# Kernel optimization log

Hardware: AMD Instinct MI355X
Metric: run time of the kernel (lower is better)

The kernel has to match this reference:

```python
import jax, jax.numpy as jnp
import numpy as np

D_MODEL = 1024
N_HEADS = 16
D_K = D_MODEL // N_HEADS
NEG = -1e9


def setup_inputs() -> dict:
    key = jax.random.key(0)
    ks = jax.random.split(key, 10)
    B, S = 4, 2048
    x = jax.random.normal(ks[0], (B, S, D_MODEL), dtype=jnp.float32)
    mask = jax.random.randint(ks[1], (B, S, S), 0, 2).astype(jnp.bool_)
    sc = 1.0 / np.sqrt(D_MODEL)
    Wq = jax.random.normal(ks[2], (D_MODEL, D_MODEL), dtype=jnp.float32) * sc
    bq = jnp.zeros((D_MODEL,), dtype=jnp.float32)
    Wk = jax.random.normal(ks[3], (D_MODEL, D_MODEL), dtype=jnp.float32) * sc
    bk = jnp.zeros((D_MODEL,), dtype=jnp.float32)
    Wv = jax.random.normal(ks[4], (D_MODEL, D_MODEL), dtype=jnp.float32) * sc
    bv = jnp.zeros((D_MODEL,), dtype=jnp.float32)
    Wo = jax.random.normal(ks[5], (D_MODEL, D_MODEL), dtype=jnp.float32) * sc
    bo = jnp.zeros((D_MODEL,), dtype=jnp.float32)
    return {"x": x, "mask": mask, "Wq": Wq, "bq": bq, "Wk": Wk, "bk": bk,
            "Wv": Wv, "bv": bv, "Wo": Wo, "bo": bo}


def _split_heads(t, B, S):
    # [B,S,d_model] -> [B,H,S,d_k]
    return t.reshape(B, S, N_HEADS, D_K).transpose(0, 2, 1, 3)


def reference(x, mask, Wq, bq, Wk, bk, Wv, bv, Wo, bo):
    B, S, _ = x.shape
    Q = _split_heads(x @ Wq + bq, B, S)
    K = _split_heads(x @ Wk + bk, B, S)
    V = _split_heads(x @ Wv + bv, B, S)
    scale = jnp.sqrt(jnp.float32(D_K))
    scores = jnp.einsum('bhqd,bhkd->bhqk', Q, K) / scale
    scores = jnp.where(mask[:, None, :, :], jnp.float32(NEG), scores)
    attn = jax.nn.softmax(scores, axis=-1)
    ctx = jnp.einsum('bhqk,bhkd->bhqd', attn, V)
    ctx = ctx.transpose(0, 2, 1, 3).reshape(B, S, D_MODEL)
    return ctx @ Wo + bo
```

## Files before the change

### kernel.cpp

```cpp
#include <hip/hip_runtime.h>

#define D_MODEL 1024
#define N_HEADS 16
#define D_K     64
#define BATCH   4
#define SEQ     2048
#define MROWS   (BATCH * SEQ)
#define QSCALE  0.18033688011112042f

typedef __bf16 bf16x8 __attribute__((ext_vector_type(8)));
typedef float  f32x4  __attribute__((ext_vector_type(4)));
typedef float  f32x16 __attribute__((ext_vector_type(16)));
typedef unsigned short ushort8 __attribute__((ext_vector_type(8)));
typedef unsigned short ushort4v __attribute__((ext_vector_type(4)));

#if __has_builtin(__builtin_amdgcn_exp2f)
#define EXP2F(x) __builtin_amdgcn_exp2f(x)
#else
#define EXP2F(x) exp2f(x)
#endif

#define CVT_PK_BF16(d, a, b) \
    asm("v_cvt_pk_bf16_f32 %0, %1, %2" : "=v"(d) : "v"(a), "v"(b))
#define PERMSWAP(a, b) \
    asm("v_permlane32_swap_b32 %0, %1" : "+v"(a), "+v"(b))
#define WAIT_VM(N) asm volatile("s_waitcnt vmcnt(" #N ")" ::: "memory")
#define CFENCE()   asm volatile("" ::: "memory")

__device__ inline unsigned short f2bf(float f) {
    union { float f; unsigned int u; } v; v.f = f;
    unsigned int u = v.u;
    unsigned int r = (u + 0x7fffu + ((u >> 16) & 1u)) >> 16;
    return (unsigned short)r;
}

__device__ inline void load_lds16(const void* g, void* l) {
    __builtin_amdgcn_global_load_lds(
        (const __attribute__((address_space(1))) unsigned int*)g,
        (__attribute__((address_space(3))) unsigned int*)l, 16, 0, 0);
}

__global__ __launch_bounds__(256) void wprep(const float* __restrict__ Wq,
                                             const float* __restrict__ Wk,
                                             const float* __restrict__ Wv,
                                             const float* __restrict__ Wo,
                                             unsigned short* __restrict__ wt) {
    __shared__ __align__(16) unsigned short t[64][65];
    int w  = blockIdx.z;
    const float* W = (w == 0) ? Wq : (w == 1) ? Wk : (w == 2) ? Wv : Wo;
    int k0 = blockIdx.x * 64, n0 = blockIdx.y * 64;
    int tid = threadIdx.x;
    int nl = tid & 63, kq = tid >> 6;
#pragma unroll
    for (int i = 0; i < 16; i++) {
        int kl = kq * 16 + i;
        t[kl][nl] = f2bf(W[(size_t)(k0 + kl) * D_MODEL + n0 + nl]);
    }
    __syncthreads();
    unsigned short* out = wt + (size_t)w * D_MODEL * D_MODEL;
#pragma unroll
    for (int p = 0; p < 2; p++) {
        int nrow = p * 32 + (tid >> 3);
        int c8   = (tid & 7) * 8;
        ushort8 o;
#pragma unroll
        for (int j = 0; j < 8; j++) o[j] = t[c8 + j][nrow];
        *reinterpret_cast<ushort8*>(out + (size_t)(n0 + nrow) * D_MODEL + k0 + c8) = o;
    }
}

__global__ __launch_bounds__(256) void xprep(const float4* __restrict__ x,
                                             unsigned short* __restrict__ xb) {
    int i = blockIdx.x * 256 + threadIdx.x;
    float4 v = x[i];
    ushort4v o;
    o[0] = f2bf(v.x); o[1] = f2bf(v.y); o[2] = f2bf(v.z); o[3] = f2bf(v.w);
    *reinterpret_cast<ushort4v*>(xb + (size_t)i * 4) = o;
}

__global__ __launch_bounds__(256) void mprep(const int* __restrict__ mask,
                                             unsigned long long* __restrict__ mb) {
    int row = blockIdx.x;
    int tid = threadIdx.x;
    int wv  = tid >> 6;
#pragma unroll
    for (int w = 0; w < 8; w++) {
        int col = w * 256 + tid;
        int mval = mask[(size_t)row * SEQ + col];
        unsigned long long bits = __ballot(mval != 0);
        if ((tid & 63) == 0) mb[(size_t)row * 32 + w * 4 + wv] = bits;
    }
}

__global__ __launch_bounds__(256) void qkv_gemm(const unsigned short* __restrict__ xb,
                                                const unsigned short* __restrict__ wt,
                                                const float* __restrict__ bq,
                                                const float* __restrict__ bk,
                                                const float* __restrict__ bvv,
                                                unsigned short* __restrict__ qb,
                                                unsigned short* __restrict__ kb,
                                                unsigned short* __restrict__ vt) {
    __shared__ __align__(16) unsigned short lds_a[128 * 32];
    __shared__ __align__(16) unsigned short lds_b[128 * 32];
    int tid = threadIdx.x;
    int wave = tid >> 6, lane = tid & 63;
    int c = lane & 15, g = lane >> 4;
    int wave_m = (wave & 1) * 64, wave_n = (wave >> 1) * 64;
    int nblk = blockIdx.x * 128, mblk = blockIdx.y * 128;

    int oct0 = wave * 128 + lane, oct1 = oct0 + 64;
    int ra0 = oct0 >> 2, ga0 = ((oct0 & 3) ^ (ra0 & 3)) * 8;
    int ra1 = oct1 >> 2, ga1 = ((oct1 & 3) ^ (ra1 & 3)) * 8;
    const unsigned short* pa0 = xb + (size_t)(mblk + ra0) * D_MODEL + ga0;
    const unsigned short* pa1 = xb + (size_t)(mblk + ra1) * D_MODEL + ga1;
    const unsigned short* pb0 = wt + (size_t)(nblk + ra0) * D_MODEL + ga0;
    const unsigned short* pb1 = wt + (size_t)(nblk + ra1) * D_MODEL + ga1;
    unsigned short* la0 = lds_a + wave * 1024;
    unsigned short* la1 = la0 + 512;
    unsigned short* lb0 = lds_b + wave * 1024;
    unsigned short* lb1 = lb0 + 512;

    int aoff[4], boff[4];
#pragma unroll
    for (int mi = 0; mi < 4; mi++) {
        int row = wave_m + mi * 16 + c;
        aoff[mi] = (row * 4 + (g ^ (row & 3))) * 16;
    }
#pragma unroll
    for (int ni = 0; ni < 4; ni++) {
        int row = wave_n + ni * 16 + c;
        boff[ni] = (row * 4 + (g ^ (row & 3))) * 16;
    }

    f32x4 acc[4][4];
#pragma unroll
    for (int mi = 0; mi < 4; mi++)
#pragma unroll
        for (int ni = 0; ni < 4; ni++) acc[mi][ni] = f32x4{0.f, 0.f, 0.f, 0.f};

    for (int k0 = 0; k0 < D_MODEL; k0 += 32) {
        load_lds16(pa0 + k0, la0);
        load_lds16(pa1 + k0, la1);
        load_lds16(pb0 + k0, lb0);
        load_lds16(pb1 + k0, lb1);
        __syncthreads();
        bf16x8 af[4], bfr[4];
#pragma unroll
        for (int mi = 0; mi < 4; mi++)
            af[mi] = *reinterpret_cast<const bf16x8*>(reinterpret_cast<const char*>(lds_a) + aoff[mi]);
#pragma unroll
        for (int ni = 0; ni < 4; ni++)
            bfr[ni] = *reinterpret_cast<const bf16x8*>(reinterpret_cast<const char*>(lds_b) + boff[ni]);
#pragma unroll
        for (int mi = 0; mi < 4; mi++)
#pragma unroll
            for (int ni = 0; ni < 4; ni++)
                acc[mi][ni] = __builtin_amdgcn_mfma_f32_16x16x32_bf16(af[mi], bfr[ni], acc[mi][ni], 0, 0, 0);
        __syncthreads();
    }

    int nb = nblk + wave_n;
    int wsel = nb >> 10;
    int h = (nb >> 6) & 15;
    int dk0 = nb & 63;
    int mglob = mblk + wave_m;
    int b = mglob >> 11;
    int s0 = mglob & (SEQ - 1);
    size_t bh = (size_t)(b * N_HEADS + h);
    const float* bias = (wsel == 0) ? bq : (wsel == 1) ? bk : bvv;
    int nn = nb & (D_MODEL - 1);
    float bval[4];
#pragma unroll
    for (int ni = 0; ni < 4; ni++) bval[ni] = bias[nn + ni * 16 + c];
    float oscale = (wsel == 0) ? QSCALE : 1.0f;

    if (wsel < 2) {
        unsigned short* outp = wsel ? kb : qb;
#pragma unroll
        for (int mi = 0; mi < 4; mi++)
#pragma unroll
            for (int ni = 0; ni < 4; ni++) {
                int dk = dk0 + ni * 16 + c;
#pragma unroll
                for (int r = 0; r < 4; r++) {
                    int s = s0 + mi * 16 + g * 4 + r;
                    outp[(bh * SEQ + s) * 64 + dk] = f2bf((acc[mi][ni][r] + bval[ni]) * oscale);
                }
            }
    } else {
#pragma unroll
        for (int mi = 0; mi < 4; mi++)
#pragma unroll
            for (int ni = 0; ni < 4; ni++) {
                int dk = dk0 + ni * 16 + c;
                int s = s0 + mi * 16 + g * 4;
                ushort4v o;
#pragma unroll
                for (int r = 0; r < 4; r++) o[r] = f2bf(acc[mi][ni][r] + bval[ni]);
                *reinterpret_cast<ushort4v*>(vt + (bh * 64 + dk) * SEQ + s) = o;
            }
    }
}

__global__ __launch_bounds__(128, 2) void attn(const unsigned short* __restrict__ qb,
                                               const unsigned short* __restrict__ kb,
                                               const unsigned short* __restrict__ vt,
                                               const unsigned long long* __restrict__ mb,
                                               unsigned short* __restrict__ ctx) {
    __shared__ __align__(16) unsigned char smem[32768];

    int tid = threadIdx.x;
    int wave = tid >> 6, lane = tid & 63;
    int q31 = lane & 31, hi = lane >> 5;
    int bh = blockIdx.x >> 4;
    int q0 = (blockIdx.x & 15) * 128 + wave * 64;
    int b = bh >> 4, h = bh & 15;
    const unsigned short* qbase = qb + (size_t)bh * SEQ * 64;
    const unsigned short* kbase = kb + (size_t)bh * SEQ * 64;
    const unsigned short* vbase = vt + (size_t)bh * 64 * SEQ;
    const unsigned long long* mp0 = mb + ((size_t)b * SEQ + q0 + q31) * 32;
    const unsigned long long* mp1 = mp0 + 1024;

    bf16x8 qf[2][4];
#pragma unroll
    for (int t = 0; t < 2; t++) {
        const unsigned short* qr = qbase + (size_t)(q0 + 32 * t + q31) * 64 + hi * 8;
#pragma unroll
        for (int c = 0; c < 4; c++)
            qf[t][c] = *reinterpret_cast<const bf16x8*>(qr + c * 16);
    }

    int srow = lane >> 3;
    int soct = (lane & 7) ^ srow;
    const unsigned short* ksrc[4];
    const unsigned short* vsrc[4];
    int stg[4];
#pragma unroll
    for (int i = 0; i < 4; i++) {
        int rbase = 16 * i + 8 * wave;
        ksrc[i] = kbase + (size_t)(rbase + srow) * 64 + soct * 8;
        vsrc[i] = vbase + (size_t)(rbase + srow) * SEQ + soct * 8;
        stg[i]  = rbase * 128;
    }

    int kofs[2][4];
#pragma unroll
    for (int s = 0; s < 2; s++)
#pragma unroll
        for (int c = 0; c < 4; c++)
            kofs[s][c] = (32 * s + q31) * 128 + (((hi + 2 * c) ^ (q31 & 7)) * 16);

    float lsum[2] = {0.f, 0.f};
    f32x16 po[2][2];
#pragma unroll
    for (int i = 0; i < 16; i++) {
        po[0][0][i] = 0.f; po[0][1][i] = 0.f;
        po[1][0][i] = 0.f; po[1][1][i] = 0.f;
    }

    unsigned long long mnx0 = mp0[0], mnx1 = mp1[0];
    CFENCE();
#pragma unroll
    for (int i = 0; i < 4; i++) {
        load_lds16(ksrc[i], smem + stg[i]);
        load_lds16(vsrc[i], smem + 8192 + stg[i]);
    }

    for (int it = 0; it < SEQ / 64; it++) {
        unsigned long long w64[2];
        w64[0] = mnx0; w64[1] = mnx1;
        int itn = (it + 1 < SEQ / 64) ? it + 1 : it;
        mnx0 = mp0[itn]; mnx1 = mp1[itn];
        CFENCE();
        unsigned char* bufn = smem + ((it + 1) & 1) * 16384;
#pragma unroll
        for (int i = 0; i < 4; i++) {
            load_lds16(ksrc[i] + itn * 4096, bufn + stg[i]);
            load_lds16(vsrc[i] + itn * 64,  bufn + 8192 + stg[i]);
        }
        WAIT_VM(10);
        __builtin_amdgcn_s_barrier();
        CFENCE();

        const char* lkb = (const char*)(smem + (it & 1) * 16384);
        const char* lvb = lkb + 8192;

#pragma unroll
        for (int s = 0; s < 2; s++) {
            f32x16 sq[2];
#pragma unroll
            for (int i = 0; i < 16; i++) { sq[0][i] = 0.f; sq[1][i] = 0.f; }
#pragma unroll
            for (int c = 0; c < 4; c++) {
                bf16x8 kf = *reinterpret_cast<const bf16x8*>(lkb + kofs[s][c]);
                sq[0] = __builtin_amdgcn_mfma_f32_32x32x16_bf16(kf, qf[0][c], sq[0], 0, 0, 0);
                sq[1] = __builtin_amdgcn_mfma_f32_32x32x16_bf16(kf, qf[1][c], sq[1], 0, 0, 0);
            }
            union PF { uint4 u; bf16x8 v; };
            PF pf[2][2];
#pragma unroll
            for (int t = 0; t < 2; t++) {
                unsigned int wt_ = ~(unsigned int)(w64[t] >> (32 * s));
                float pm[16];
#pragma unroll
                for (int j = 0; j < 4; j++) {
                    unsigned int nj = wt_ >> (8 * j + 4 * hi);
#pragma unroll
                    for (int e = 0; e < 4; e++) {
                        float p = EXP2F(sq[t][4 * j + e]);
                        unsigned int m = (unsigned int)((int)(nj << (31 - e)) >> 31);
                        unsigned int pu = __float_as_uint(p) & m;
                        pm[4 * j + e] = __uint_as_float(pu);
                        lsum[t] += __uint_as_float(pu);
                    }
                }
                unsigned int w[8];
#pragma unroll
                for (int j = 0; j < 4; j++) {
                    CVT_PK_BF16(w[2 * j],     pm[4 * j + 0], pm[4 * j + 1]);
                    CVT_PK_BF16(w[2 * j + 1], pm[4 * j + 2], pm[4 * j + 3]);
                }
                PERMSWAP(w[0], w[2]); PERMSWAP(w[1], w[3]);
                PERMSWAP(w[4], w[6]); PERMSWAP(w[5], w[7]);
                pf[t][0].u = uint4{w[0], w[1], w[2], w[3]};
                pf[t][1].u = uint4{w[4], w[5], w[6], w[7]};
            }
#pragma unroll
            for (int cp = 0; cp < 2; cp++) {
                int c = 2 * s + cp;
#pragma unroll
                for (int so = 0; so < 2; so++) {
                    bf16x8 vf = *reinterpret_cast<const bf16x8*>(lvb + kofs[so][c]);
                    po[0][so] = __builtin_amdgcn_mfma_f32_32x32x16_bf16(vf, pf[0][cp].v, po[0][so], 0, 0, 0);
                    po[1][so] = __builtin_amdgcn_mfma_f32_32x32x16_bf16(vf, pf[1][cp].v, po[1][so], 0, 0, 0);
                }
            }
        }
        CFENCE();
        __builtin_amdgcn_s_barrier();
    }

    WAIT_VM(0);
    __builtin_amdgcn_s_barrier();

    float inv[2];
#pragma unroll
    for (int t = 0; t < 2; t++) {
        lsum[t] += __shfl_xor(lsum[t], 32);
        inv[t] = 1.f / lsum[t];
    }

    unsigned int* ob = (unsigned int*)(smem + wave * 8192);
    int csw = 4 * (q31 & 7);
#pragma unroll
    for (int t = 0; t < 2; t++) {
        unsigned int* obr = ob + (32 * t + q31) * 32;
#pragma unroll
        for (int so = 0; so < 2; so++)
#pragma unroll
            for (int j = 0; j < 4; j++) {
                unsigned int w0 = (unsigned int)f2bf(po[t][so][4 * j + 0] * inv[t])
                                | ((unsigned int)f2bf(po[t][so][4 * j + 1] * inv[t]) << 16);
                unsigned int w1 = (unsigned int)f2bf(po[t][so][4 * j + 2] * inv[t])
                                | ((unsigned int)f2bf(po[t][so][4 * j + 3] * inv[t]) << 16);
                int d = (16 * so + 4 * j + 2 * hi) ^ csw;
                uint2 u; u.x = w0; u.y = w1;
                *reinterpret_cast<uint2*>(obr + d) = u;
            }
    }
    __builtin_amdgcn_s_waitcnt(0);
    size_t crow = (size_t)b * SEQ + q0;
    int o = lane & 7, rl = lane >> 3;
#pragma unroll
    for (int i = 0; i < 8; i++) {
        int r = 8 * i + rl;
        uint4 v = *reinterpret_cast<const uint4*>(ob + r * 32 + 4 * (o ^ (r & 7)));
        *reinterpret_cast<uint4*>(ctx + (crow + r) * D_MODEL + h * 64 + o * 8) = v;
    }
}

__global__ __launch_bounds__(256) void oproj(const unsigned short* __restrict__ ctx,
                                             const unsigned short* __restrict__ wt,
                                             const float* __restrict__ bo,
                                             float* __restrict__ out) {
    __shared__ __align__(16) unsigned short lds_a[128 * 32];
    __shared__ __align__(16) unsigned short lds_b[128 * 32];
    int tid = threadIdx.x;
    int wave = tid >> 6, lane = tid & 63;
    int c = lane & 15, g = lane >> 4;
    int wave_m = (wave & 1) * 64, wave_n = (wave >> 1) * 64;
    int nblk = blockIdx.x * 128, mblk = blockIdx.y * 128;
    const unsigned short* wo = wt + (size_t)3 * D_MODEL * D_MODEL;

    int oct0 = wave * 128 + lane, oct1 = oct0 + 64;
    int ra0 = oct0 >> 2, ga0 = ((oct0 & 3) ^ (ra0 & 3)) * 8;
    int ra1 = oct1 >> 2, ga1 = ((oct1 & 3) ^ (ra1 & 3)) * 8;
    const unsigned short* pa0 = ctx + (size_t)(mblk + ra0) * D_MODEL + ga0;
    const unsigned short* pa1 = ctx + (size_t)(mblk + ra1) * D_MODEL + ga1;
    const unsigned short* pb0 = wo + (size_t)(nblk + ra0) * D_MODEL + ga0;
    const unsigned short* pb1 = wo + (size_t)(nblk + ra1) * D_MODEL + ga1;
    unsigned short* la0 = lds_a + wave * 1024;
    unsigned short* la1 = la0 + 512;
    unsigned short* lb0 = lds_b + wave * 1024;
    unsigned short* lb1 = lb0 + 512;

    int aoff[4], boff[4];
#pragma unroll
    for (int mi = 0; mi < 4; mi++) {
        int row = wave_m + mi * 16 + c;
        aoff[mi] = (row * 4 + (g ^ (row & 3))) * 16;
    }
#pragma unroll
    for (int ni = 0; ni < 4; ni++) {
        int row = wave_n + ni * 16 + c;
        boff[ni] = (row * 4 + (g ^ (row & 3))) * 16;
    }

    f32x4 acc[4][4];
#pragma unroll
    for (int mi = 0; mi < 4; mi++)
#pragma unroll
        for (int ni = 0; ni < 4; ni++) acc[mi][ni] = f32x4{0.f, 0.f, 0.f, 0.f};

    for (int k0 = 0; k0 < D_MODEL; k0 += 32) {
        load_lds16(pa0 + k0, la0);
        load_lds16(pa1 + k0, la1);
        load_lds16(pb0 + k0, lb0);
        load_lds16(pb1 + k0, lb1);
        __syncthreads();
        bf16x8 af[4], bfr[4];
#pragma unroll
        for (int mi = 0; mi < 4; mi++)
            af[mi] = *reinterpret_cast<const bf16x8*>(reinterpret_cast<const char*>(lds_a) + aoff[mi]);
#pragma unroll
        for (int ni = 0; ni < 4; ni++)
            bfr[ni] = *reinterpret_cast<const bf16x8*>(reinterpret_cast<const char*>(lds_b) + boff[ni]);
#pragma unroll
        for (int mi = 0; mi < 4; mi++)
#pragma unroll
            for (int ni = 0; ni < 4; ni++)
                acc[mi][ni] = __builtin_amdgcn_mfma_f32_16x16x32_bf16(af[mi], bfr[ni], acc[mi][ni], 0, 0, 0);
        __syncthreads();
    }

    float bval[4];
#pragma unroll
    for (int ni = 0; ni < 4; ni++) bval[ni] = bo[nblk + wave_n + ni * 16 + c];
#pragma unroll
    for (int mi = 0; mi < 4; mi++)
#pragma unroll
        for (int ni = 0; ni < 4; ni++) {
            int n = nblk + wave_n + ni * 16 + c;
#pragma unroll
            for (int r = 0; r < 4; r++) {
                int m = mblk + wave_m + mi * 16 + g * 4 + r;
                out[(size_t)m * D_MODEL + n] = acc[mi][ni][r] + bval[ni];
            }
        }
}

extern "C" void kernel_launch(void* const* d_in, const int* in_sizes, int n_in,
                              void* d_out, int out_size, void* d_ws, size_t ws_size,
                              hipStream_t stream) {
    const float* x    = (const float*)d_in[0];
    const int*   mask = (const int*)d_in[1];
    const float* Wq = (const float*)d_in[2];
    const float* bq = (const float*)d_in[3];
    const float* Wk = (const float*)d_in[4];
    const float* bk = (const float*)d_in[5];
    const float* Wv = (const float*)d_in[6];
    const float* bv = (const float*)d_in[7];
    const float* Wo = (const float*)d_in[8];
    const float* bo = (const float*)d_in[9];
    float* out = (float*)d_out;

    char* ws = (char*)d_ws;
    const size_t MB = 1024 * 1024;
    unsigned short* wt  = (unsigned short*)(ws + 0 * MB);
    unsigned short* xb  = (unsigned short*)(ws + 8 * MB);
    unsigned short* qb  = (unsigned short*)(ws + 24 * MB);
    unsigned short* kb  = (unsigned short*)(ws + 40 * MB);
    unsigned short* vt  = (unsigned short*)(ws + 56 * MB);
    unsigned short* ctx = (unsigned short*)(ws + 72 * MB);
    unsigned long long* mb = (unsigned long long*)(ws + 88 * MB);

    wprep<<<dim3(16, 16, 4), 256, 0, stream>>>(Wq, Wk, Wv, Wo, wt);
    xprep<<<dim3(MROWS * D_MODEL / 4 / 256), 256, 0, stream>>>((const float4*)x, xb);
    mprep<<<dim3(MROWS), 256, 0, stream>>>(mask, mb);
    qkv_gemm<<<dim3(24, 64), 256, 0, stream>>>(xb, wt, bq, bk, bv, qb, kb, vt);
    attn<<<dim3(1024), 128, 0, stream>>>(qb, kb, vt, mb, ctx);
    oproj<<<dim3(8, 64), 256, 0, stream>>>(ctx, wt, bo, out);
}
```

Baseline: 363.9 us.

## Use single-wave attention blocks with 32-key tiles and XCD-aware block swizzling

Attention blocks become one wave each (64 threads), walking 32-key tiles with a double-buffered LDS stage. Because no other wave shares the LDS, the workgroup barriers are gone, and s_setprio raises priority around the MFMA sections. All three main kernels now take a 1D grid whose block index is remapped so that consecutive blocks on the same XCD (stride 8) touch neighbouring tiles or heads, aiming at better L2 reuse. The trade-offs are twice as many loop iterations with per-iteration overhead, and K/V tiles are no longer shared between two waves, so global loads double.

Measured after the change: 366.5 us. No clear change (+0.7%).

```diff
diff --git a/kernel.cpp b/kernel.cpp
--- a/kernel.cpp
+++ b/kernel.cpp
@@ -106,7 +106,9 @@
     int wave = tid >> 6, lane = tid & 63;
     int c = lane & 15, g = lane >> 4;
     int wave_m = (wave & 1) * 64, wave_n = (wave >> 1) * 64;
-    int nblk = blockIdx.x * 128, mblk = blockIdx.y * 128;
+    int wg = blockIdx.x;
+    int swz = (wg & 7) * 192 + (wg >> 3);
+    int nblk = (swz % 24) * 128, mblk = (swz / 24) * 128;
 
     int oct0 = wave * 128 + lane, oct1 = oct0 + 64;
     int ra0 = oct0 >> 2, ga0 = ((oct0 & 3) ^ (ra0 & 3)) * 8;
@@ -202,24 +204,25 @@
     }
 }
 
-__global__ __launch_bounds__(128, 2) void attn(const unsigned short* __restrict__ qb,
-                                               const unsigned short* __restrict__ kb,
-                                               const unsigned short* __restrict__ vt,
-                                               const unsigned long long* __restrict__ mb,
-                                               unsigned short* __restrict__ ctx) {
-    __shared__ __align__(16) unsigned char smem[32768];
-
-    int tid = threadIdx.x;
-    int wave = tid >> 6, lane = tid & 63;
+__global__ __launch_bounds__(64, 2) void attn(const unsigned short* __restrict__ qb,
+                                              const unsigned short* __restrict__ kb,
+                                              const unsigned short* __restrict__ vt,
+                                              const unsigned long long* __restrict__ mb,
+                                              unsigned short* __restrict__ ctx) {
+    __shared__ __align__(16) unsigned char smem[16384];
+
+    int lane = threadIdx.x;
     int q31 = lane & 31, hi = lane >> 5;
-    int bh = blockIdx.x >> 4;
-    int q0 = (blockIdx.x & 15) * 128 + wave * 64;
+    int bid = blockIdx.x;
+    int swz = (bid & 7) * 256 + (bid >> 3);
+    int bh = swz >> 5;
+    int q0 = (swz & 31) * 64;
     int b = bh >> 4, h = bh & 15;
     const unsigned short* qbase = qb + (size_t)bh * SEQ * 64;
     const unsigned short* kbase = kb + (size_t)bh * SEQ * 64;
     const unsigned short* vbase = vt + (size_t)bh * 64 * SEQ;
-    const unsigned long long* mp0 = mb + ((size_t)b * SEQ + q0 + q31) * 32;
-    const unsigned long long* mp1 = mp0 + 1024;
+    const unsigned int* mp0 = (const unsigned int*)mb + ((size_t)b * SEQ + q0 + q31) * 64;
+    const unsigned int* mp1 = mp0 + 32 * 64;
 
     bf16x8 qf[2][4];
 #pragma unroll
@@ -230,25 +233,27 @@
             qf[t][c] = *reinterpret_cast<const bf16x8*>(qr + c * 16);
     }
 
-    int srow = lane >> 3;
-    int soct = (lane & 7) ^ srow;
+    int srow8 = lane >> 3;
+    int j7 = lane & 7;
+    int soct = j7 ^ srow8;
     const unsigned short* ksrc[4];
     const unsigned short* vsrc[4];
-    int stg[4];
 #pragma unroll
     for (int i = 0; i < 4; i++) {
-        int rbase = 16 * i + 8 * wave;
-        ksrc[i] = kbase + (size_t)(rbase + srow) * 64 + soct * 8;
-        vsrc[i] = vbase + (size_t)(rbase + srow) * SEQ + soct * 8;
-        stg[i]  = rbase * 128;
-    }
-
-    int kofs[2][4];
-#pragma unroll
-    for (int s = 0; s < 2; s++)
-#pragma unroll
-        for (int c = 0; c < 4; c++)
-            kofs[s][c] = (32 * s + q31) * 128 + (((hi + 2 * c) ^ (q31 & 7)) * 16);
+        ksrc[i] = kbase + (size_t)(8 * i + srow8) * 64 + soct * 8;
+        vsrc[i] = vbase + (size_t)(8 * i + srow8 + ((soct >> 2) << 5)) * SEQ + (soct & 3) * 8;
+    }
+
+    int kofs[4];
+#pragma unroll
+    for (int c = 0; c < 4; c++)
+        kofs[c] = q31 * 128 + (((hi + 2 * c) ^ (q31 & 7)) * 16);
+    int vofs[2][2];
+#pragma unroll
+    for (int so = 0; so < 2; so++)
+#pragma unroll
+        for (int cp = 0; cp < 2; cp++)
+            vofs[so][cp] = q31 * 128 + (((4 * so + hi + 2 * cp) ^ (q31 & 7)) * 16);
 
     float lsum[2] = {0.f, 0.f};
     f32x16 po[2][2];
@@ -258,90 +263,85 @@
         po[1][0][i] = 0.f; po[1][1][i] = 0.f;
     }
 
-    unsigned long long mnx0 = mp0[0], mnx1 = mp1[0];
+    unsigned int mnx0 = mp0[0], mnx1 = mp1[0];
     CFENCE();
 #pragma unroll
     for (int i = 0; i < 4; i++) {
-        load_lds16(ksrc[i], smem + stg[i]);
-        load_lds16(vsrc[i], smem + 8192 + stg[i]);
-    }
-
-    for (int it = 0; it < SEQ / 64; it++) {
-        unsigned long long w64[2];
-        w64[0] = mnx0; w64[1] = mnx1;
-        int itn = (it + 1 < SEQ / 64) ? it + 1 : it;
+        load_lds16(ksrc[i], smem + i * 1024);
+        load_lds16(vsrc[i], smem + 4096 + i * 1024);
+    }
+
+    for (int it = 0; it < SEQ / 32; it++) {
+        unsigned int w32[2];
+        w32[0] = mnx0; w32[1] = mnx1;
+        int itn = (it + 1 < SEQ / 32) ? it + 1 : it;
         mnx0 = mp0[itn]; mnx1 = mp1[itn];
         CFENCE();
-        unsigned char* bufn = smem + ((it + 1) & 1) * 16384;
+        unsigned char* bufn = smem + ((it + 1) & 1) * 8192;
 #pragma unroll
         for (int i = 0; i < 4; i++) {
-            load_lds16(ksrc[i] + itn * 4096, bufn + stg[i]);
-            load_lds16(vsrc[i] + itn * 64,  bufn + 8192 + stg[i]);
+            load_lds16(ksrc[i] + (size_t)itn * 2048, bufn + i * 1024);
+            load_lds16(vsrc[i] + itn * 32, bufn + 4096 + i * 1024);
         }
         WAIT_VM(10);
-        __builtin_amdgcn_s_barrier();
         CFENCE();
 
-        const char* lkb = (const char*)(smem + (it & 1) * 16384);
-        const char* lvb = lkb + 8192;
-
-#pragma unroll
-        for (int s = 0; s < 2; s++) {
-            f32x16 sq[2];
-#pragma unroll
-            for (int i = 0; i < 16; i++) { sq[0][i] = 0.f; sq[1][i] = 0.f; }
-#pragma unroll
-            for (int c = 0; c < 4; c++) {
-                bf16x8 kf = *reinterpret_cast<const bf16x8*>(lkb + kofs[s][c]);
-                sq[0] = __builtin_amdgcn_mfma_f32_32x32x16_bf16(kf, qf[0][c], sq[0], 0, 0, 0);
-                sq[1] = __builtin_amdgcn_mfma_f32_32x32x16_bf16(kf, qf[1][c], sq[1], 0, 0, 0);
-            }
-            union PF { uint4 u; bf16x8 v; };
-            PF pf[2][2];
-#pragma unroll
-            for (int t = 0; t < 2; t++) {
-                unsigned int wt_ = ~(unsigned int)(w64[t] >> (32 * s));
-                float pm[16];
-#pragma unroll
-                for (int j = 0; j < 4; j++) {
-                    unsigned int nj = wt_ >> (8 * j + 4 * hi);
-#pragma unroll
-                    for (int e = 0; e < 4; e++) {
-                        float p = EXP2F(sq[t][4 * j + e]);
-                        unsigned int m = (unsigned int)((int)(nj << (31 - e)) >> 31);
-                        unsigned int pu = __float_as_uint(p) & m;
-                        pm[4 * j + e] = __uint_as_float(pu);
-                        lsum[t] += __uint_as_float(pu);
-                    }
+        const char* lkb = (const char*)(smem + (it & 1) * 8192);
+        const char* lvb = lkb + 4096;
+
+        f32x16 sq[2];
+#pragma unroll
+        for (int i = 0; i < 16; i++) { sq[0][i] = 0.f; sq[1][i] = 0.f; }
+        __builtin_amdgcn_s_setprio(1);
+#pragma unroll
+        for (int c = 0; c < 4; c++) {
+            bf16x8 kf = *reinterpret_cast<const bf16x8*>(lkb + kofs[c]);
+            sq[0] = __builtin_amdgcn_mfma_f32_32x32x16_bf16(kf, qf[0][c], sq[0], 0, 0, 0);
+            sq[1] = __builtin_amdgcn_mfma_f32_32x32x16_bf16(kf, qf[1][c], sq[1], 0, 0, 0);
+        }
+        __builtin_amdgcn_s_setprio(0);
+        union PF { uint4 u; bf16x8 v; };
+        PF pf[2][2];
+#pragma unroll
+        for (int t = 0; t < 2; t++) {
+            unsigned int wt_ = ~w32[t];
+            float pm[16];
+#pragma unroll
+            for (int j = 0; j < 4; j++) {
+                unsigned int nj = wt_ >> (8 * j + 4 * hi);
+#pragma unroll
+                for (int e = 0; e < 4; e++) {
+                    float p = EXP2F(sq[t][4 * j + e]);
+                    unsigned int m = (unsigned int)((int)(nj << (31 - e)) >> 31);
+                    unsigned int pu = __float_as_uint(p) & m;
+                    pm[4 * j + e] = __uint_as_float(pu);
+                    lsum[t] += __uint_as_float(pu);
                 }
-                unsigned int w[8];
-#pragma unroll
-                for (int j = 0; j < 4; j++) {
-                    CVT_PK_BF16(w[2 * j],     pm[4 * j + 0], pm[4 * j + 1]);
-                    CVT_PK_BF16(w[2 * j + 1], pm[4 * j + 2], pm[4 * j + 3]);
-                }
-                PERMSWAP(w[0], w[2]); PERMSWAP(w[1], w[3]);
-                PERMSWAP(w[4], w[6]); PERMSWAP(w[5], w[7]);
-                pf[t][0].u = uint4{w[0], w[1], w[2], w[3]};
-                pf[t][1].u = uint4{w[4], w[5], w[6], w[7]};
-            }
-#pragma unroll
-            for (int cp = 0; cp < 2; cp++) {
-                int c = 2 * s + cp;
-#pragma unroll
-                for (int so = 0; so < 2; so++) {
-                    bf16x8 vf = *reinterpret_cast<const bf16x8*>(lvb + kofs[so][c]);
-                    po[0][so] = __builtin_amdgcn_mfma_f32_32x32x16_bf16(vf, pf[0][cp].v, po[0][so], 0, 0, 0);
-                    po[1][so] = __builtin_amdgcn_mfma_f32_32x32x16_bf16(vf, pf[1][cp].v, po[1][so], 0, 0, 0);
-                }
-            }
+            }
+            unsigned int w[8];
+#pragma unroll
+            for (int j = 0; j < 4; j++) {
+                CVT_PK_BF16(w[2 * j],     pm[4 * j + 0], pm[4 * j + 1]);
+                CVT_PK_BF16(w[2 * j + 1], pm[4 * j + 2], pm[4 * j + 3]);
+            }
+            PERMSWAP(w[0], w[2]); PERMSWAP(w[1], w[3]);
+            PERMSWAP(w[4], w[6]); PERMSWAP(w[5], w[7]);
+            pf[t][0].u = uint4{w[0], w[1], w[2], w[3]};
+            pf[t][1].u = uint4{w[4], w[5], w[6], w[7]};
         }
-        CFENCE();
-        __builtin_amdgcn_s_barrier();
+        __builtin_amdgcn_s_setprio(1);
+#pragma unroll
+        for (int cp = 0; cp < 2; cp++)
+#pragma unroll
+            for (int so = 0; so < 2; so++) {
+                bf16x8 vf = *reinterpret_cast<const bf16x8*>(lvb + vofs[so][cp]);
+                po[0][so] = __builtin_amdgcn_mfma_f32_32x32x16_bf16(vf, pf[0][cp].v, po[0][so], 0, 0, 0);
+                po[1][so] = __builtin_amdgcn_mfma_f32_32x32x16_bf16(vf, pf[1][cp].v, po[1][so], 0, 0, 0);
+            }
+        __builtin_amdgcn_s_setprio(0);
     }
 
     WAIT_VM(0);
-    __builtin_amdgcn_s_barrier();
 
     float inv[2];
 #pragma unroll
@@ -350,7 +350,7 @@
         inv[t] = 1.f / lsum[t];
     }
 
-    unsigned int* ob = (unsigned int*)(smem + wave * 8192);
+    unsigned int* ob = (unsigned int*)smem;
     int csw = 4 * (q31 & 7);
 #pragma unroll
     for (int t = 0; t < 2; t++) {
@@ -389,7 +389,9 @@
     int wave = tid >> 6, lane = tid & 63;
     int c = lane & 15, g = lane >> 4;
     int wave_m = (wave & 1) * 64, wave_n = (wave >> 1) * 64;
-    int nblk = blockIdx.x * 128, mblk = blockIdx.y * 128;
+    int wg = blockIdx.x;
+    int swz = (wg & 7) * 64 + (wg >> 3);
+    int nblk = (swz & 7) * 128, mblk = (swz >> 3) * 128;
     const unsigned short* wo = wt + (size_t)3 * D_MODEL * D_MODEL;
 
     int oct0 = wave * 128 + lane, oct1 = oct0 + 64;
@@ -487,7 +489,7 @@
     wprep<<<dim3(16, 16, 4), 256, 0, stream>>>(Wq, Wk, Wv, Wo, wt);
     xprep<<<dim3(MROWS * D_MODEL / 4 / 256), 256, 0, stream>>>((const float4*)x, xb);
     mprep<<<dim3(MROWS), 256, 0, stream>>>(mask, mb);
-    qkv_gemm<<<dim3(24, 64), 256, 0, stream>>>(xb, wt, bq, bk, bv, qb, kb, vt);
-    attn<<<dim3(1024), 128, 0, stream>>>(qb, kb, vt, mb, ctx);
-    oproj<<<dim3(8, 64), 256, 0, stream>>>(ctx, wt, bo, out);
-}
+    qkv_gemm<<<dim3(1536), 256, 0, stream>>>(xb, wt, bq, bk, bv, qb, kb, vt);
+    attn<<<dim3(2048), 64, 0, stream>>>(qb, kb, vt, mb, ctx);
+    oproj<<<dim3(512), 256, 0, stream>>>(ctx, wt, bo, out);
+}
```
